# Kernel tuning notes

Measured on AMD Instinct MI355X. Metric: run time of the kernel, lower is better.

## Reference

```python
import jax, jax.numpy as jnp
import numpy as np

B, C, HW, A, E, H1, HID = 4096, 4, 64, 32, 4, 1024, 512


def setup_inputs() -> dict:
    key = jax.random.key(0)
    ks = jax.random.split(key, 16)
    def rn(k, shape, fan_in):
        return jax.random.normal(k, shape, dtype=jnp.float32) / np.sqrt(fan_in)
    inp = {
        "x": jax.random.normal(ks[0], (B, C, HW, HW), dtype=jnp.float32),
        # conv stack (OIHW)
        "cW1": rn(ks[1], (32, C, 8, 8), C * 64), "cb1": 0.1 * jnp.ones((32,), jnp.float32),
        "cW2": rn(ks[2], (64, 32, 4, 4), 32 * 16), "cb2": 0.1 * jnp.ones((64,), jnp.float32),
        "cW3": rn(ks[3], (64, 64, 3, 3), 64 * 9), "cb3": 0.1 * jnp.ones((64,), jnp.float32),
        # E expert advantage streams: Linear(1024->512), relu, Linear(512->A)
        "aW1": rn(ks[4], (E, H1, HID), H1), "ab1": jnp.zeros((E, HID), jnp.float32),
        "aW2": rn(ks[5], (E, HID, A), HID), "ab2": jnp.zeros((E, A), jnp.float32),
        # E expert value streams: Linear(1024->512), relu, Linear(512->1)
        "vW1": rn(ks[6], (E, H1, HID), H1), "vb1": jnp.zeros((E, HID), jnp.float32),
        "vW2": rn(ks[7], (E, HID, 1), HID), "vb2": jnp.zeros((E, 1), jnp.float32),
        # reward bucket boundaries (buffer): boundaries * scale - 1e-8
        "boundaries": jnp.array([-0.5, 0.0, 0.5], jnp.float32) * 1.0 - 1e-8,
    }
    return inp


def _conv(h, W, b, stride):
    out = jax.lax.conv_general_dilated(h, W, (stride, stride), "VALID",
                                       dimension_numbers=("NCHW", "OIHW", "NCHW"))
    return out + b[None, :, None, None]


def _routed_mlp(h, W1, b1, W2, b2, idx):
    # h: [B, H1]; W1: [E, H1, HID]; W2: [E, HID, O]; idx: [B]
    # Compute all experts (E is tiny), then gather the routed output per sample.
    z = jax.nn.relu(jnp.einsum("bi,eio->ebo", h, W1) + b1[:, None, :])  # [E,B,HID]
    y = jnp.einsum("ebo,eoa->eba", z, W2) + b2[:, None, :]              # [E,B,O]
    return y[idx, jnp.arange(h.shape[0])]                                # [B,O]


def reference(x, cW1, cb1, cW2, cb2, cW3, cb3, aW1, ab1, aW2, ab2,
              vW1, vb1, vW2, vb2, boundaries):
    h = jax.nn.relu(_conv(x, cW1, cb1, 4))   # [B,32,15,15]
    h = jax.nn.relu(_conv(h, cW2, cb2, 2))   # [B,64,6,6]
    h = jax.nn.relu(_conv(h, cW3, cb3, 1))   # [B,64,4,4]
    bsz = x.shape[0]
    h = h.reshape(bsz, -1)                   # [B,1024]
    rewards = x[:, -1, 0, 0]                 # [B]
    idx = jnp.sum(rewards[:, None] > boundaries[None, :], axis=1)  # [B] in [0,E)
    ya = _routed_mlp(h, aW1, ab1, aW2, ab2, idx)  # [B,A]
    mean = jnp.sum(ya, axis=1, keepdims=True) / ya.shape[1]
    ys = _routed_mlp(h, vW1, vb1, vW2, vb2, idx)  # [B,1]
    q = (ya - mean) + ys
    return q
```

## Files before the change

kernel.cpp:

```cpp
#include <hip/hip_runtime.h>
#include <hip/hip_bf16.h>

typedef __bf16 bf16;
typedef bf16 bf16x8 __attribute__((ext_vector_type(8)));
typedef bf16 bf16x4 __attribute__((ext_vector_type(4)));
typedef float f32x4 __attribute__((ext_vector_type(4)));

__device__ __forceinline__ int SZ(int a) { return a ^ (((a >> 7) & 7) << 4); }

__global__ __launch_bounds__(256) void k_pre(const float* __restrict__ cW1,
    const float* __restrict__ cW2, const float* __restrict__ cW3,
    bf16* __restrict__ W1p, bf16* __restrict__ W2p, bf16* __restrict__ W3p) {
  const int bid = blockIdx.x, tid = threadIdx.x;
  if (bid < 32) {
    int i = bid * 256 + tid;
    int oc = i >> 8, k = i & 255;
    int ic = k & 3, kp = k >> 2, kx = kp & 7, ky = kp >> 3;
    W1p[i] = (bf16)cW1[oc * 256 + ic * 64 + ky * 8 + kx];
  } else if (bid < 160) {
    int i = (bid - 32) * 256 + tid;
    int oc = i >> 9, k = i & 511;
    int ic = k & 31, kp = k >> 5, kx = kp & 3, ky = kp >> 2;
    W2p[i] = (bf16)cW2[oc * 512 + ic * 16 + ky * 4 + kx];
  } else {
    int i = (bid - 160) * 256 + tid;
    if (i < 36864) {
      int oc = i / 576, k = i - oc * 576;
      int ic = k & 63, kp = k >> 6, kx = kp % 3, ky = kp / 3;
      W3p[i] = (bf16)cW3[oc * 576 + ic * 9 + ky * 3 + kx];
    }
  }
}

__global__ __launch_bounds__(256) void k_pre2(const float* __restrict__ aW1,
    const float* __restrict__ vW1, bf16* __restrict__ W1T) {
  __shared__ float t[64][65];
  const int bid2 = blockIdx.x;
  const int bz = bid2 >> 7, rest = bid2 & 127, by = rest >> 4, bx = rest & 15;
  const float* in = (bz >= 4 ? vW1 : aW1) + (size_t)(bz & 3) * 524288;
  const int k0 = bx * 64, n0 = by * 64;
  const int tid = threadIdx.x, cc = tid & 63, r0 = (tid >> 6) * 16;
  for (int i = 0; i < 16; ++i)
    t[r0 + i][cc] = in[(size_t)(k0 + r0 + i) * 512 + n0 + cc];
  __syncthreads();
  for (int i = 0; i < 16; ++i) {
    int n = r0 + i, k = cc;
    W1T[((size_t)bz * 512 + n0 + n) * 1024 + k0 + k] = (bf16)t[k][n];
  }
}

__global__ __launch_bounds__(1024) void k_route(const float* __restrict__ x,
    const float* __restrict__ bd, int* __restrict__ perm, int* __restrict__ cnt) {
  const int tid = threadIdx.x;
  const float t0 = bd[0], t1 = bd[1], t2 = bd[2];
  int e[4];
  #pragma unroll
  for (int i = 0; i < 4; ++i) {
    const int b = tid * 4 + i;
    const float r = x[(size_t)b * 16384 + 12288];
    e[i] = (r > t0) + (r > t1) + (r > t2);
  }
  int lc[4] = {0, 0, 0, 0};
  #pragma unroll
  for (int i = 0; i < 4; ++i) lc[e[i]]++;
  const int lane = tid & 63, wv = tid >> 6;
  __shared__ int wsum[16][4];
  __shared__ int wbase[16][4];
  int pre[4];
  #pragma unroll
  for (int q = 0; q < 4; ++q) {
    int v = lc[q];
    #pragma unroll
    for (int d = 1; d < 64; d <<= 1) {
      int u = __shfl_up(v, d);
      if (lane >= d) v += u;
    }
    pre[q] = v - lc[q];
    if (lane == 63) wsum[wv][q] = v;
  }
  __syncthreads();
  if (tid == 0) {
    int tot[4] = {0, 0, 0, 0};
    for (int w = 0; w < 16; ++w)
      #pragma unroll
      for (int q = 0; q < 4; ++q) { wbase[w][q] = tot[q]; tot[q] += wsum[w][q]; }
    #pragma unroll
    for (int q = 0; q < 4; ++q) cnt[q] = tot[q];
  }
  __syncthreads();
  int run[4];
  #pragma unroll
  for (int q = 0; q < 4; ++q) run[q] = wbase[wv][q] + pre[q];
  #pragma unroll
  for (int i = 0; i < 4; ++i) {
    const int b = tid * 4 + i;
    perm[e[i] * 4096 + run[e[i]]] = b;
    run[e[i]]++;
  }
}

__global__ __launch_bounds__(256, 3) void k_conv123(const float* __restrict__ x,
    const bf16* __restrict__ W1p, const float* __restrict__ b1,
    const bf16* __restrict__ W2p, const float* __restrict__ b2,
    const bf16* __restrict__ W3p, const float* __restrict__ b3,
    bf16* __restrict__ h3) {
  __shared__ bf16 sA[16384];
  __shared__ bf16 sh1[9000];
  const int b = blockIdx.x, tid = threadIdx.x;
  const int lane = tid & 63, wave = tid >> 6, lid = lane & 15, c = lane >> 4;

  {
    bf16x8 bw[8];
    const int ot = wave & 1, col = ot * 16 + lid;
    #pragma unroll
    for (int ks = 0; ks < 8; ++ks) bw[ks] = *(const bf16x8*)(W1p + col * 256 + ks * 32 + c * 8);
    const float bias = b1[col];
    #pragma unroll
    for (int ks = 0; ks < 8; ++ks) asm volatile("" : "+v"(bw[ks]));

    const float4* xs = (const float4*)(x + (size_t)b * 16384);
    #pragma unroll
    for (int hb = 0; hb < 2; ++hb) {
      float4 r[2][4];
      #pragma unroll
      for (int h = 0; h < 2; ++h)
        #pragma unroll
        for (int ic = 0; ic < 4; ++ic)
          r[h][ic] = xs[ic * 1024 + tid + (hb * 2 + h) * 256];
      #pragma unroll
      for (int h = 0; h < 2; ++h) {
        const int g = tid + (hb * 2 + h) * 256;
        bf16x8 lo, hi;
        lo[0] = (bf16)r[h][0].x; lo[1] = (bf16)r[h][1].x; lo[2] = (bf16)r[h][2].x; lo[3] = (bf16)r[h][3].x;
        lo[4] = (bf16)r[h][0].y; lo[5] = (bf16)r[h][1].y; lo[6] = (bf16)r[h][2].y; lo[7] = (bf16)r[h][3].y;
        hi[0] = (bf16)r[h][0].z; hi[1] = (bf16)r[h][1].z; hi[2] = (bf16)r[h][2].z; hi[3] = (bf16)r[h][3].z;
        hi[4] = (bf16)r[h][0].w; hi[5] = (bf16)r[h][1].w; hi[6] = (bf16)r[h][2].w; hi[7] = (bf16)r[h][3].w;
        *(bf16x8*)((char*)sA + SZ(g * 32))      = lo;
        *(bf16x8*)((char*)sA + SZ(g * 32 + 16)) = hi;
      }
    }
    __syncthreads();

    int ab[8], ptv[8];
    #pragma unroll
    for (int pi = 0; pi < 8; ++pi) {
      int pt = (wave >> 1) + 2 * pi; if (pt > 14) pt = 14;
      ptv[pi] = pt;
      int p = pt * 16 + lid; if (p > 224) p = 224;
      const int py = p / 15, px = p - py * 15;
      ab[pi] = py * 2048 + px * 32 + c * 16;
    }
    f32x4 acc[8];
    #pragma unroll
    for (int pi = 0; pi < 8; ++pi) acc[pi] = (f32x4){0.f, 0.f, 0.f, 0.f};
    #pragma unroll
    for (int ks = 0; ks < 8; ++ks)
      #pragma unroll
      for (int pi = 0; pi < 8; ++pi)
        acc[pi] = __builtin_amdgcn_mfma_f32_16x16x32_bf16(
            *(const bf16x8*)((const char*)sA + SZ(ab[pi] + ks * 512)), bw[ks], acc[pi], 0, 0, 0);
    __syncthreads();
    #pragma unroll
    for (int pi = 0; pi < 8; ++pi)
      #pragma unroll
      for (int r = 0; r < 4; ++r) {
        const int pr = ptv[pi] * 16 + c * 4 + r;
        if (pr < 225) sh1[pr * 40 + col] = (bf16)fmaxf(acc[pi][r] + bias, 0.f);
      }
  }
  __syncthreads();

  bf16* sh2 = sA;
  const int col = wave * 16 + lid;
  {
    bf16x8 bw2[16];
    #pragma unroll
    for (int ks = 0; ks < 16; ++ks) bw2[ks] = *(const bf16x8*)(W2p + col * 512 + ks * 32 + c * 8);
    const float bias2 = b2[col];
    #pragma unroll
    for (int ks = 0; ks < 16; ++ks) asm volatile("" : "+v"(bw2[ks]));

    int abase[3];
    #pragma unroll
    for (int pt = 0; pt < 3; ++pt) {
      int p = pt * 16 + lid; if (p > 35) p = 35;
      const int oy = p / 6, ox = p - oy * 6;
      abase[pt] = (oy * 30 + ox * 2) * 40 + c * 8;
    }
    f32x4 acc2[3];
    #pragma unroll
    for (int pt = 0; pt < 3; ++pt) acc2[pt] = (f32x4){0.f, 0.f, 0.f, 0.f};
    #pragma unroll
    for (int ks = 0; ks < 16; ++ks) {
      const int ky = ks >> 2, kx = ks & 3;
      #pragma unroll
      for (int pt = 0; pt < 3; ++pt)
        acc2[pt] = __builtin_amdgcn_mfma_f32_16x16x32_bf16(
            *(const bf16x8*)(&sh1[abase[pt] + (ky * 15 + kx) * 40]), bw2[ks], acc2[pt], 0, 0, 0);
    }
    #pragma unroll
    for (int pt = 0; pt < 3; ++pt)
      #pragma unroll
      for (int r = 0; r < 4; ++r) {
        const int pr = pt * 16 + c * 4 + r;
        if (pr < 36) sh2[pr * 72 + col] = (bf16)fmaxf(acc2[pt][r] + bias2, 0.f);
      }
  }
  __syncthreads();

  {
    bf16x8 bw3[18];
    #pragma unroll
    for (int ks = 0; ks < 18; ++ks) bw3[ks] = *(const bf16x8*)(W3p + col * 576 + ks * 32 + c * 8);
    const float bias3 = b3[col];
    #pragma unroll
    for (int ks = 0; ks < 18; ++ks) asm volatile("" : "+v"(bw3[ks]));
    const int oy = lid >> 2, ox = lid & 3;
    const int ab3 = (oy * 6 + ox) * 72 + c * 8;
    f32x4 acc = {0.f, 0.f, 0.f, 0.f};
    #pragma unroll
    for (int ks = 0; ks < 18; ++ks) {
      const int kp = ks >> 1, ky = kp / 3, kx = kp - ky * 3;
      acc = __builtin_amdgcn_mfma_f32_16x16x32_bf16(
          *(const bf16x8*)(&sh2[ab3 + (ky * 6 + kx) * 72 + (ks & 1) * 32]), bw3[ks], acc, 0, 0, 0);
    }
    bf16x4 o;
    #pragma unroll
    for (int r = 0; r < 4; ++r) o[r] = (bf16)fmaxf(acc[r] + bias3, 0.f);
    *(bf16x4*)(h3 + (size_t)b * 1024 + col * 16 + c * 4) = o;
  }
}

__global__ __launch_bounds__(512) void k_mlp1(const bf16* __restrict__ h3,
    const bf16* __restrict__ W1T, const float* __restrict__ ab1, const float* __restrict__ vb1,
    const int* __restrict__ perm, const int* __restrict__ cnt,
    bf16* __restrict__ za, bf16* __restrict__ zv) {
  const int e = blockIdx.z;
  const int cntE = cnt[e];
  const int m0 = blockIdx.x * 64;
  if (m0 >= cntE) return;
  const int n0 = blockIdx.y * 128;
  const bf16* WA = W1T + (size_t)e * 524288;
  const bf16* WV = W1T + (size_t)(4 + e) * 524288;

  __shared__ bf16 As[64 * 72];
  __shared__ int rows[64];
  const int tid = threadIdx.x;
  if (tid < 64) {
    int j = m0 + tid; if (j > cntE - 1) j = cntE - 1;
    rows[tid] = perm[e * 4096 + j];
  }
  __syncthreads();

  const int lane = tid & 63, wave = tid >> 6;
  const int lid = lane & 15, c = lane >> 4;
  const int wm = wave >> 2, wn = wave & 3;
  const int srow = tid >> 3, skoff = (tid & 7) * 8;
  const bf16* arow = h3 + (size_t)rows[srow] * 1024 + skoff;
  const int colA = n0 + wn * 32 + lid;
  const bf16* wa0 = WA + (size_t)colA * 1024 + c * 8;
  const bf16* wa1 = WA + (size_t)(colA + 16) * 1024 + c * 8;
  const bf16* wv0 = WV + (size_t)colA * 1024 + c * 8;
  const bf16* wv1 = WV + (size_t)(colA + 16) * 1024 + c * 8;
  const int ar0 = (wm * 32 + lid) * 72 + c * 8;
  const int ar1 = (wm * 32 + 16 + lid) * 72 + c * 8;

  f32x4 acc[2][2][2];
  #pragma unroll
  for (int n = 0; n < 2; ++n)
    #pragma unroll
    for (int m = 0; m < 2; ++m)
      #pragma unroll
      for (int f = 0; f < 2; ++f) acc[n][m][f] = (f32x4){0.f, 0.f, 0.f, 0.f};

  for (int k0 = 0; k0 < 1024; k0 += 64) {
    *(bf16x8*)(&As[srow * 72 + skoff]) = *(const bf16x8*)(arow + k0);
    __syncthreads();
    bf16x8 a[2][2];
    #pragma unroll
    for (int m = 0; m < 2; ++m)
      #pragma unroll
      for (int ks = 0; ks < 2; ++ks)
        a[m][ks] = *(const bf16x8*)(&As[(m ? ar1 : ar0) + ks * 32]);
    #pragma unroll
    for (int ks = 0; ks < 2; ++ks) {
      bf16x8 bA0 = *(const bf16x8*)(wa0 + k0 + ks * 32);
      bf16x8 bA1 = *(const bf16x8*)(wa1 + k0 + ks * 32);
      bf16x8 bV0 = *(const bf16x8*)(wv0 + k0 + ks * 32);
      bf16x8 bV1 = *(const bf16x8*)(wv1 + k0 + ks * 32);
      #pragma unroll
      for (int m = 0; m < 2; ++m) {
        acc[0][m][0] = __builtin_amdgcn_mfma_f32_16x16x32_bf16(a[m][ks], bA0, acc[0][m][0], 0, 0, 0);
        acc[0][m][1] = __builtin_amdgcn_mfma_f32_16x16x32_bf16(a[m][ks], bA1, acc[0][m][1], 0, 0, 0);
        acc[1][m][0] = __builtin_amdgcn_mfma_f32_16x16x32_bf16(a[m][ks], bV0, acc[1][m][0], 0, 0, 0);
        acc[1][m][1] = __builtin_amdgcn_mfma_f32_16x16x32_bf16(a[m][ks], bV1, acc[1][m][1], 0, 0, 0);
      }
    }
    __syncthreads();
  }

  #pragma unroll
  for (int cf = 0; cf < 2; ++cf) {
    const int col = colA + cf * 16;
    const float bA = ab1[e * 512 + col];
    const float bV = vb1[e * 512 + col];
    #pragma unroll
    for (int m = 0; m < 2; ++m)
      #pragma unroll
      for (int r = 0; r < 4; ++r) {
        const int ridx = wm * 32 + m * 16 + c * 4 + r;
        if (m0 + ridx < cntE) {
          const size_t zoff = (size_t)rows[ridx] * 512 + col;
          za[zoff] = (bf16)fmaxf(acc[0][m][cf][r] + bA, 0.f);
          zv[zoff] = (bf16)fmaxf(acc[1][m][cf][r] + bV, 0.f);
        }
      }
  }
}

__global__ __launch_bounds__(256) void k_mlp2(const bf16* __restrict__ za,
    const bf16* __restrict__ zv,
    const float* __restrict__ aW2, const float* __restrict__ ab2,
    const float* __restrict__ vW2, const float* __restrict__ vb2,
    const int* __restrict__ perm, const int* __restrict__ cnt,
    float* __restrict__ out) {
  const int e = blockIdx.y;
  const int cntE = cnt[e];
  const int m0 = blockIdx.x * 64;
  if (m0 >= cntE) return;
  __shared__ bf16 Bs[48 * 520];
  const int tid = threadIdx.x;
  for (int i = tid; i < 512 * 32; i += 256) {
    const int k = i >> 5, n = i & 31;
    Bs[n * 520 + k] = (bf16)aW2[(size_t)e * 16384 + i];
  }
  for (int i = tid; i < 512; i += 256) Bs[32 * 520 + i] = (bf16)vW2[e * 512 + i];
  for (int i = tid; i < 15 * 512; i += 256) {
    const int n = 33 + (i >> 9), k = i & 511;
    Bs[n * 520 + k] = (bf16)0.f;
  }
  __syncthreads();

  const int lane = tid & 63, wave = tid >> 6;
  const int lid = lane & 15, c = lane >> 4;
  const int row0 = m0 + wave * 16;
  if (row0 >= cntE) return;
  int rowl = row0 + lid; if (rowl > cntE - 1) rowl = cntE - 1;
  const int pb = perm[e * 4096 + rowl];
  const bf16* aA = za + (size_t)pb * 512 + c * 8;
  const bf16* aV = zv + (size_t)pb * 512 + c * 8;

  f32x4 acc0 = {0.f, 0.f, 0.f, 0.f}, acc1 = acc0, accv = acc0;
  #pragma unroll
  for (int k0 = 0; k0 < 512; k0 += 32) {
    bf16x8 a1 = *(const bf16x8*)(aA + k0);
    bf16x8 a2 = *(const bf16x8*)(aV + k0);
    bf16x8 b0 = *(const bf16x8*)(&Bs[lid * 520 + k0 + c * 8]);
    bf16x8 b1 = *(const bf16x8*)(&Bs[(16 + lid) * 520 + k0 + c * 8]);
    bf16x8 b2 = *(const bf16x8*)(&Bs[(32 + lid) * 520 + k0 + c * 8]);
    acc0 = __builtin_amdgcn_mfma_f32_16x16x32_bf16(a1, b0, acc0, 0, 0, 0);
    acc1 = __builtin_amdgcn_mfma_f32_16x16x32_bf16(a1, b1, acc1, 0, 0, 0);
    accv = __builtin_amdgcn_mfma_f32_16x16x32_bf16(a2, b2, accv, 0, 0, 0);
  }

  const float ba0 = ab2[e * 32 + lid], ba1 = ab2[e * 32 + 16 + lid], bv = vb2[e];
  #pragma unroll
  for (int r = 0; r < 4; ++r) {
    const int row = row0 + c * 4 + r;
    const float y0 = acc0[r] + ba0, y1 = acc1[r] + ba1;
    float s = y0 + y1;
    s += __shfl_xor(s, 1); s += __shfl_xor(s, 2);
    s += __shfl_xor(s, 4); s += __shfl_xor(s, 8);
    const float mean = s * 0.03125f;
    const float ys = __shfl(accv[r], lane & 48) + bv;
    if (row < cntE) {
      const int bq = perm[e * 4096 + row];
      out[(size_t)bq * 32 + lid] = y0 - mean + ys;
      out[(size_t)bq * 32 + 16 + lid] = y1 - mean + ys;
    }
  }
}

extern "C" void kernel_launch(void* const* d_in, const int* in_sizes, int n_in,
                              void* d_out, int out_size, void* d_ws, size_t ws_size,
                              hipStream_t stream) {
  const float* x   = (const float*)d_in[0];
  const float* cW1 = (const float*)d_in[1];
  const float* cb1 = (const float*)d_in[2];
  const float* cW2 = (const float*)d_in[3];
  const float* cb2 = (const float*)d_in[4];
  const float* cW3 = (const float*)d_in[5];
  const float* cb3 = (const float*)d_in[6];
  const float* aW1 = (const float*)d_in[7];
  const float* ab1 = (const float*)d_in[8];
  const float* aW2 = (const float*)d_in[9];
  const float* ab2 = (const float*)d_in[10];
  const float* vW1 = (const float*)d_in[11];
  const float* vb1 = (const float*)d_in[12];
  const float* vW2 = (const float*)d_in[13];
  const float* vb2 = (const float*)d_in[14];
  const float* bd  = (const float*)d_in[15];
  float* out = (float*)d_out;

  char* ws = (char*)d_ws;
  bf16* W1T = (bf16*)(ws);
  bf16* za  = (bf16*)(ws + 8388608ull);
  bf16* zv  = (bf16*)(ws + 12582912ull);
  bf16* h3  = (bf16*)(ws + 16777216ull);
  bf16* W1p = (bf16*)(ws + 25165824ull);
  bf16* W2p = (bf16*)(ws + 25182208ull);
  bf16* W3p = (bf16*)(ws + 25247744ull);
  int* perm = (int*)(ws + 25321472ull);
  int* cnt  = (int*)(ws + 25387008ull);

  k_pre<<<304, 256, 0, stream>>>(cW1, cW2, cW3, W1p, W2p, W3p);
  k_pre2<<<1024, 256, 0, stream>>>(aW1, vW1, W1T);
  k_route<<<1, 1024, 0, stream>>>(x, bd, perm, cnt);
  k_conv123<<<4096, 256, 0, stream>>>(x, W1p, cb1, W2p, cb2, W3p, cb3, h3);
  k_mlp1<<<dim3(64, 4, 4), 512, 0, stream>>>(h3, W1T, ab1, vb1, perm, cnt, za, zv);
  k_mlp2<<<dim3(64, 4), 256, 0, stream>>>(za, zv, aW2, ab2, vW2, vb2, perm, cnt, out);
}
```

Baseline: 207.4 us.

## Feed conv1 MFMA operands directly from global x, dropping LDS staging

The first convolution no longer stages the fp32 input image into a swizzled bf16 LDS buffer. Each lane now loads its 8-wide operand fragments straight from global memory as float4 pairs and converts them to bf16 inline. The conv1 weights are repacked in their natural OIHW order so the K dimension lines up with contiguous kx runs. Freeing the 32 KB staging buffer and one barrier allows the occupancy hint to rise from 3 to 4 blocks per CU. In exchange, overlapping input windows are re-read through L1/L2 and re-converted several times, and conv1 now depends on many more global loads in flight.

```diff
diff --git a/kernel.cpp b/kernel.cpp
--- a/kernel.cpp
+++ b/kernel.cpp
@@ -5,8 +5,6 @@
 typedef bf16 bf16x8 __attribute__((ext_vector_type(8)));
 typedef bf16 bf16x4 __attribute__((ext_vector_type(4)));
 typedef float f32x4 __attribute__((ext_vector_type(4)));
-
-__device__ __forceinline__ int SZ(int a) { return a ^ (((a >> 7) & 7) << 4); }
 
 __global__ __launch_bounds__(256) void k_pre(const float* __restrict__ cW1,
     const float* __restrict__ cW2, const float* __restrict__ cW3,
@@ -14,9 +12,7 @@
   const int bid = blockIdx.x, tid = threadIdx.x;
   if (bid < 32) {
     int i = bid * 256 + tid;
-    int oc = i >> 8, k = i & 255;
-    int ic = k & 3, kp = k >> 2, kx = kp & 7, ky = kp >> 3;
-    W1p[i] = (bf16)cW1[oc * 256 + ic * 64 + ky * 8 + kx];
+    W1p[i] = (bf16)cW1[i];
   } else if (bid < 160) {
     int i = (bid - 32) * 256 + tid;
     int oc = i >> 9, k = i & 511;
@@ -99,67 +95,51 @@
   }
 }
 
-__global__ __launch_bounds__(256, 3) void k_conv123(const float* __restrict__ x,
+__global__ __launch_bounds__(256, 4) void k_conv123(const float* __restrict__ x,
     const bf16* __restrict__ W1p, const float* __restrict__ b1,
     const bf16* __restrict__ W2p, const float* __restrict__ b2,
     const bf16* __restrict__ W3p, const float* __restrict__ b3,
     bf16* __restrict__ h3) {
-  __shared__ bf16 sA[16384];
   __shared__ bf16 sh1[9000];
+  __shared__ bf16 sh2[2592];
   const int b = blockIdx.x, tid = threadIdx.x;
   const int lane = tid & 63, wave = tid >> 6, lid = lane & 15, c = lane >> 4;
 
   {
+    const int ot = wave & 1, col = ot * 16 + lid;
     bf16x8 bw[8];
-    const int ot = wave & 1, col = ot * 16 + lid;
     #pragma unroll
     for (int ks = 0; ks < 8; ++ks) bw[ks] = *(const bf16x8*)(W1p + col * 256 + ks * 32 + c * 8);
     const float bias = b1[col];
     #pragma unroll
     for (int ks = 0; ks < 8; ++ks) asm volatile("" : "+v"(bw[ks]));
 
-    const float4* xs = (const float4*)(x + (size_t)b * 16384);
-    #pragma unroll
-    for (int hb = 0; hb < 2; ++hb) {
-      float4 r[2][4];
-      #pragma unroll
-      for (int h = 0; h < 2; ++h)
-        #pragma unroll
-        for (int ic = 0; ic < 4; ++ic)
-          r[h][ic] = xs[ic * 1024 + tid + (hb * 2 + h) * 256];
-      #pragma unroll
-      for (int h = 0; h < 2; ++h) {
-        const int g = tid + (hb * 2 + h) * 256;
-        bf16x8 lo, hi;
-        lo[0] = (bf16)r[h][0].x; lo[1] = (bf16)r[h][1].x; lo[2] = (bf16)r[h][2].x; lo[3] = (bf16)r[h][3].x;
-        lo[4] = (bf16)r[h][0].y; lo[5] = (bf16)r[h][1].y; lo[6] = (bf16)r[h][2].y; lo[7] = (bf16)r[h][3].y;
-        hi[0] = (bf16)r[h][0].z; hi[1] = (bf16)r[h][1].z; hi[2] = (bf16)r[h][2].z; hi[3] = (bf16)r[h][3].z;
-        hi[4] = (bf16)r[h][0].w; hi[5] = (bf16)r[h][1].w; hi[6] = (bf16)r[h][2].w; hi[7] = (bf16)r[h][3].w;
-        *(bf16x8*)((char*)sA + SZ(g * 32))      = lo;
-        *(bf16x8*)((char*)sA + SZ(g * 32 + 16)) = hi;
-      }
-    }
-    __syncthreads();
-
-    int ab[8], ptv[8];
+    const float* xb = x + (size_t)b * 16384;
+    int abase[8], ptv[8];
     #pragma unroll
     for (int pi = 0; pi < 8; ++pi) {
       int pt = (wave >> 1) + 2 * pi; if (pt > 14) pt = 14;
       ptv[pi] = pt;
       int p = pt * 16 + lid; if (p > 224) p = 224;
       const int py = p / 15, px = p - py * 15;
-      ab[pi] = py * 2048 + px * 32 + c * 16;
+      abase[pi] = py * 256 + px * 4;
     }
     f32x4 acc[8];
     #pragma unroll
     for (int pi = 0; pi < 8; ++pi) acc[pi] = (f32x4){0.f, 0.f, 0.f, 0.f};
     #pragma unroll
-    for (int ks = 0; ks < 8; ++ks)
-      #pragma unroll
-      for (int pi = 0; pi < 8; ++pi)
-        acc[pi] = __builtin_amdgcn_mfma_f32_16x16x32_bf16(
-            *(const bf16x8*)((const char*)sA + SZ(ab[pi] + ks * 512)), bw[ks], acc[pi], 0, 0, 0);
-    __syncthreads();
+    for (int ks = 0; ks < 8; ++ks) {
+      const int off = (ks >> 1) * 4096 + ((ks & 1) * 4 + c) * 64;
+      #pragma unroll
+      for (int pi = 0; pi < 8; ++pi) {
+        const float4 lo = *(const float4*)(xb + off + abase[pi]);
+        const float4 hi = *(const float4*)(xb + off + abase[pi] + 4);
+        bf16x8 a;
+        a[0] = (bf16)lo.x; a[1] = (bf16)lo.y; a[2] = (bf16)lo.z; a[3] = (bf16)lo.w;
+        a[4] = (bf16)hi.x; a[5] = (bf16)hi.y; a[6] = (bf16)hi.z; a[7] = (bf16)hi.w;
+        acc[pi] = __builtin_amdgcn_mfma_f32_16x16x32_bf16(a, bw[ks], acc[pi], 0, 0, 0);
+      }
+    }
     #pragma unroll
     for (int pi = 0; pi < 8; ++pi)
       #pragma unroll
@@ -170,7 +150,6 @@
   }
   __syncthreads();
 
-  bf16* sh2 = sA;
   const int col = wave * 16 + lid;
   {
     bf16x8 bw2[16];
```

Measured after the change: 285.4 us. 37.6% more time.
